# Kernel tuning notes

Measured on AMD Instinct MI355X. Metric: run time of the kernel, lower is better.

The kernel has to match this reference:

```python
import jax, jax.numpy as jnp
import numpy as np

HID = 128
H = 96
W = 96
WS = 6      # window_size
SS = 3      # shift_size
LN_EPS = 1e-5


def _layer_norm(x, g, b):
    m = x.mean(-1, keepdims=True)
    v = ((x - m) ** 2).mean(-1, keepdims=True)
    return (x - m) / jnp.sqrt(v + LN_EPS) * g + b


def _block(x, Wm, bm, g, bg):
    # Linear -> LayerNorm -> GELU (dropout is identity at inference)
    return jax.nn.gelu(_layer_norm(x @ Wm + bm, g, bg), approximate=False)


def _window_context(grid, Wt, bt, gt, bgt):
    # grid: [B, H, W, D]. Window partition + mean over the ws*ws tokens is
    # equivalent to a mean over each (ws, ws) tile; broadcasting back is a repeat.
    B, Hh, Ww, D = grid.shape
    nh, nw = Hh // WS, Ww // WS
    win_mean = grid.reshape(B, nh, WS, nw, WS, D).mean(axis=(2, 4))  # [B, nh, nw, D]
    tok = _block(win_mean, Wt, bt, gt, bgt)                          # token_proj
    return jnp.repeat(jnp.repeat(tok, WS, axis=1), WS, axis=2)       # [B, H, W, D]


def setup_inputs() -> dict:
    key = jax.random.key(0)
    ks = jax.random.split(key, 8)
    B = 32
    s = 1.0 / np.sqrt(HID)
    inp = {
        "h_pixel": jax.random.normal(ks[0], (B, H * W, HID), dtype=jnp.float32),
        "node_mask": jnp.ones((B, H * W), dtype=jnp.float32),
        # token_proj: Linear(D,D) + LayerNorm(D)
        "Wt": jax.random.normal(ks[1], (HID, HID), dtype=jnp.float32) * s,
        "bt": jnp.zeros((HID,), jnp.float32),
        "gt": jnp.ones((HID,), jnp.float32),
        "bgt": jnp.zeros((HID,), jnp.float32),
        # fuse: Linear(D,D) + LayerNorm(D)  (regular_shifted_sum -> fuse_in = D)
        "Wf": jax.random.normal(ks[2], (HID, HID), dtype=jnp.float32) * s,
        "bf": jnp.zeros((HID,), jnp.float32),
        "gf": jnp.ones((HID,), jnp.float32),
        "bgf": jnp.zeros((HID,), jnp.float32),
        # out_proj: Linear(D,D) + LayerNorm(D)
        "Wo": jax.random.normal(ks[3], (HID, HID), dtype=jnp.float32) * s,
        "bo": jnp.zeros((HID,), jnp.float32),
        "go": jnp.ones((HID,), jnp.float32),
        "bgo": jnp.zeros((HID,), jnp.float32),
    }
    return inp


def reference(h_pixel, node_mask, Wt, bt, gt, bgt, Wf, bf, gf, bgf, Wo, bo, go, bgo):
    B, N, D = h_pixel.shape
    grid = h_pixel.reshape(B, H, W, D)
    reg = _window_context(grid, Wt, bt, gt, bgt)
    shifted = jnp.roll(grid, (-SS, -SS), axis=(1, 2))
    sh = _window_context(shifted, Wt, bt, gt, bgt)
    sh = jnp.roll(sh, (SS, SS), axis=(1, 2))
    ctx = _block(reg + sh, Wf, bf, gf, bgf)     # fuse
    out = _block(ctx, Wo, bo, go, bgo)          # out_proj
    out = out.reshape(B, N, D) * node_mask[..., None]
    return out
```

## Files before the change

kernel.cpp:

```cpp
#include <hip/hip_runtime.h>
#include <hip/hip_bf16.h>


#define DEVFN static __device__ __forceinline__

typedef __attribute__((ext_vector_type(8))) short bf16x8;
typedef __attribute__((ext_vector_type(16))) float f32x16;
typedef __attribute__((ext_vector_type(2))) unsigned int uintx2;
typedef __attribute__((ext_vector_type(4))) float floatx4;

DEVFN float gelu_fast(float x) {
  const float u = 1.5957691216057308f * (x + 0.044715f * x * x * x);
  return x / (1.0f + __expf(-u));
}

DEVFN unsigned int cvt_pk_bf16(float lo, float hi) {
  unsigned int r;
  asm("v_cvt_pk_bf16_f32 %0, %1, %2" : "=v"(r) : "v"(lo), "v"(hi));
  return r;
}

DEVFN float bf2f(unsigned short u) {
  return __uint_as_float((unsigned int)u << 16);
}

DEVFN void add4(float4& a, const float4 v) {
  a.x += v.x; a.y += v.y; a.z += v.z; a.w += v.w;
}
DEVFN void fma4(float4& a, const float4 v, float m) {
  a.x = fmaf(v.x, m, a.x); a.y = fmaf(v.y, m, a.y);
  a.z = fmaf(v.z, m, a.z); a.w = fmaf(v.w, m, a.w);
}

__global__ __launch_bounds__(512) void k_tile3(const float* __restrict__ h,
                                               unsigned short* __restrict__ S3) {
  const int b  = blockIdx.x >> 5;
  const int ry = blockIdx.x & 31;
  const int w    = threadIdx.x >> 6;
  const int lane = threadIdx.x & 63;
  const int half = lane >> 5;
  const int ch4  = (lane & 31) << 2;
  const float mlo = half ? 0.f : 1.f;
  const float mhi = 1.f - mlo;

  float4 acc[4];
  #pragma unroll
  for (int t = 0; t < 4; ++t) acc[t] = make_float4(0.f, 0.f, 0.f, 0.f);

  #pragma unroll
  for (int yy = 0; yy < 3; ++yy) {
    const float* rp =
        h + ((size_t)(b * 9216 + (3 * ry + yy) * 96 + 12 * w + half) * 128 + ch4);
    #pragma unroll
    for (int j = 0; j < 6; ++j) {
      const float4 v = *reinterpret_cast<const float4*>(rp + j * 256);
      if (j == 0)      add4(acc[0], v);
      else if (j == 2) add4(acc[1], v);
      else if (j == 3) add4(acc[2], v);
      else if (j == 5) add4(acc[3], v);
      else if (j == 1) { fma4(acc[0], v, mlo); fma4(acc[1], v, mhi); }
      else             { fma4(acc[2], v, mlo); fma4(acc[3], v, mhi); }
    }
  }

  #pragma unroll
  for (int t = 0; t < 4; ++t) {
    float4 s = acc[t];
    s.x += __shfl_xor(s.x, 32, 64);
    s.y += __shfl_xor(s.y, 32, 64);
    s.z += __shfl_xor(s.z, 32, 64);
    s.w += __shfl_xor(s.w, 32, 64);
    if (half == 0) {
      uintx2 pk;
      pk.x = cvt_pk_bf16(s.x, s.y);
      pk.y = cvt_pk_bf16(s.z, s.w);
      __builtin_nontemporal_store(pk, reinterpret_cast<uintx2*>(
          &S3[((size_t)(b * 32 + ry) * 32 + 4 * w + t) * 128 + ch4]));
    }
  }
}

DEVFN void stage_w_bf(unsigned short* __restrict__ wl,
                      const float* __restrict__ W, int tid) {
  #pragma unroll
  for (int p = 0; p < 4; ++p) {
    const int i = tid + p * 512;
    const int kp = i >> 5;
    const int n4 = (i & 31) * 4;
    const float4 r0 = *reinterpret_cast<const float4*>(W + (size_t)(2 * kp) * 128 + n4);
    const float4 r1 = *reinterpret_cast<const float4*>(W + (size_t)(2 * kp + 1) * 128 + n4);
    const float a0[4] = {r0.x, r0.y, r0.z, r0.w};
    const float a1[4] = {r1.x, r1.y, r1.z, r1.w};
    #pragma unroll
    for (int j = 0; j < 4; ++j) {
      *reinterpret_cast<unsigned int*>(&wl[(n4 + j) * 136 + 2 * kp]) =
          cvt_pk_bf16(a0[j], a1[j]);
    }
  }
}

DEVFN f32x16 mfma_tile(const unsigned short* __restrict__ xrow,
                       const unsigned short* __restrict__ wrow) {
  f32x16 acc;
  #pragma unroll
  for (int r = 0; r < 16; ++r) acc[r] = 0.f;
  #pragma unroll
  for (int kk = 0; kk < 8; ++kk) {
    const bf16x8 a = *reinterpret_cast<const bf16x8*>(xrow + kk * 16);
    const bf16x8 bb = *reinterpret_cast<const bf16x8*>(wrow + kk * 16);
    acc = __builtin_amdgcn_mfma_f32_32x32x16_bf16(a, bb, acc, 0, 0, 0);
  }
  return acc;
}

DEVFN void write_raw(float* __restrict__ raw, const f32x16 acc,
                     int tg, int cg, int lane) {
  const int n  = cg * 32 + (lane & 31);
  const int mb = tg * 32 + 4 * (lane >> 5);
  #pragma unroll
  for (int r = 0; r < 16; ++r) {
    const int mm = mb + (r & 3) + 8 * (r >> 2);
    raw[mm * 132 + n] = acc[r];
  }
}

__global__ __launch_bounds__(512) void k_tok(const unsigned short* __restrict__ S3,
    const float* __restrict__ Wt, const float* __restrict__ bt,
    const float* __restrict__ gt, const float* __restrict__ bgt,
    unsigned short* __restrict__ tok) {
  __shared__ __align__(16) unsigned short xs_bf[64 * 136];
  __shared__ __align__(16) unsigned short wl[128 * 136];
  float* raw = reinterpret_cast<float*>(wl);

  const int tid = threadIdx.x;
  const int t0 = blockIdx.x * 64;
  const int s  = t0 >> 13;
  const int b  = (t0 >> 8) & 31;
  const int wyx = t0 & 255;

  const unsigned short* Sb = S3 + (size_t)b * 131072;
  #pragma unroll
  for (int p = 0; p < 2; ++p) {
    const int i = tid + p * 512;
    const int tt = i >> 4, c8 = (i & 15) * 8;
    const int idx = wyx + tt;
    const int wy = idx >> 4, wx = idx & 15;
    int ry0, ry1, c0, c1;
    if (s == 0) { ry0 = 2 * wy;     ry1 = 2 * wy + 1;        c0 = 2 * wx;     c1 = 2 * wx + 1; }
    else        { ry0 = 2 * wy + 1; ry1 = (2 * wy + 2) & 31; c0 = 2 * wx + 1; c1 = (2 * wx + 2) & 31; }
    const bf16x8 v00 = *reinterpret_cast<const bf16x8*>(Sb + ((size_t)(ry0 * 32 + c0) * 128 + c8));
    const bf16x8 v01 = *reinterpret_cast<const bf16x8*>(Sb + ((size_t)(ry0 * 32 + c1) * 128 + c8));
    const bf16x8 v10 = *reinterpret_cast<const bf16x8*>(Sb + ((size_t)(ry1 * 32 + c0) * 128 + c8));
    const bf16x8 v11 = *reinterpret_cast<const bf16x8*>(Sb + ((size_t)(ry1 * 32 + c1) * 128 + c8));
    float sv[8];
    #pragma unroll
    for (int j = 0; j < 8; ++j) {
      sv[j] = (bf2f((unsigned short)v00[j]) + bf2f((unsigned short)v01[j]) +
               bf2f((unsigned short)v10[j]) + bf2f((unsigned short)v11[j])) * (1.f / 36.f);
    }
    unsigned int* dst = reinterpret_cast<unsigned int*>(&xs_bf[tt * 136 + c8]);
    #pragma unroll
    for (int j = 0; j < 4; ++j)
      dst[j] = cvt_pk_bf16(sv[2 * j], sv[2 * j + 1]);
  }
  stage_w_bf(wl, Wt, tid);
  __syncthreads();

  const int lane = tid & 63;
  const int w = tid >> 6;
  const int tg = w >> 2, cg = w & 3;
  const unsigned short* xrow = &xs_bf[(tg * 32 + (lane & 31)) * 136 + 8 * (lane >> 5)];
  const unsigned short* wrow = &wl[(cg * 32 + (lane & 31)) * 136 + 8 * (lane >> 5)];

  const f32x16 acc = mfma_tile(xrow, wrow);
  __syncthreads();
  write_raw(raw, acc, tg, cg, lane);
  __syncthreads();

  {
    const int tt = tid >> 3, cb = tid & 7;
    float v[16];
    float s2 = 0.f, q = 0.f;
    #pragma unroll
    for (int i = 0; i < 4; ++i) {
      const int col = 4 * cb + 32 * i;
      const float4 rv = *reinterpret_cast<const float4*>(&raw[tt * 132 + col]);
      const float4 bv = *reinterpret_cast<const float4*>(bt + col);
      v[4 * i + 0] = rv.x + bv.x; v[4 * i + 1] = rv.y + bv.y;
      v[4 * i + 2] = rv.z + bv.z; v[4 * i + 3] = rv.w + bv.w;
    }
    #pragma unroll
    for (int e = 0; e < 16; ++e) { s2 += v[e]; q += v[e] * v[e]; }
    s2 += __shfl_xor(s2, 1, 8); q += __shfl_xor(q, 1, 8);
    s2 += __shfl_xor(s2, 2, 8); q += __shfl_xor(q, 2, 8);
    s2 += __shfl_xor(s2, 4, 8); q += __shfl_xor(q, 4, 8);
    const float mean = s2 * (1.f / 128.f);
    const float var  = q * (1.f / 128.f) - mean * mean;
    const float inv  = rsqrtf(var + 1e-5f);
    #pragma unroll
    for (int i = 0; i < 4; ++i) {
      const int col = 4 * cb + 32 * i;
      const float4 gv = *reinterpret_cast<const float4*>(gt + col);
      const float4 ev = *reinterpret_cast<const float4*>(bgt + col);
      const float o0 = gelu_fast((v[4 * i + 0] - mean) * inv * gv.x + ev.x);
      const float o1 = gelu_fast((v[4 * i + 1] - mean) * inv * gv.y + ev.y);
      const float o2 = gelu_fast((v[4 * i + 2] - mean) * inv * gv.z + ev.z);
      const float o3 = gelu_fast((v[4 * i + 3] - mean) * inv * gv.w + ev.w);
      uintx2 pk;
      pk.x = cvt_pk_bf16(o0, o1);
      pk.y = cvt_pk_bf16(o2, o3);
      __builtin_nontemporal_store(pk, reinterpret_cast<uintx2*>(
          tok + (size_t)(t0 + tt) * 128 + col));
    }
  }
}

__global__ __launch_bounds__(512) void k_fuse_out(const unsigned short* __restrict__ tok,
    const float* __restrict__ Wf, const float* __restrict__ bfv,
    const float* __restrict__ gf, const float* __restrict__ bgf,
    const float* __restrict__ Wo, const float* __restrict__ bo,
    const float* __restrict__ go, const float* __restrict__ bgo,
    const float* __restrict__ mask, float* __restrict__ out) {
  __shared__ __align__(16) unsigned short xs_bf[64 * 136];
  __shared__ __align__(16) unsigned short wl[128 * 136];
  float* raw = reinterpret_cast<float*>(wl);

  const int tid = threadIdx.x;
  const int b = blockIdx.x >> 4;
  const int m = blockIdx.x & 15;
  const int lane = tid & 63;
  const int w = tid >> 6;
  const int tg = w >> 2, cg = w & 3;

  const unsigned short* tokR = tok + (size_t)b * 32768 + (size_t)m * 2048;
  const unsigned short* tokS = tok + 1048576 + (size_t)b * 32768;

  #pragma unroll
  for (int p = 0; p < 2; ++p) {
    const int i = tid + p * 512;
    const int t = i >> 4, c8 = (i & 15) * 8;
    const int gx = t & 31, gy = 2 * m + (t >> 5);
    const int wx  = gx >> 1;
    const int wxs = ((gx + 31) & 31) >> 1;
    const int wys = ((gy + 31) & 31) >> 1;
    const bf16x8 pr = *reinterpret_cast<const bf16x8*>(tokR + (size_t)wx * 128 + c8);
    const bf16x8 ps = *reinterpret_cast<const bf16x8*>(tokS + (size_t)(wys * 16 + wxs) * 128 + c8);
    float sv[8];
    #pragma unroll
    for (int j = 0; j < 8; ++j)
      sv[j] = bf2f((unsigned short)pr[j]) + bf2f((unsigned short)ps[j]);
    unsigned int* dst = reinterpret_cast<unsigned int*>(&xs_bf[t * 136 + c8]);
    #pragma unroll
    for (int j = 0; j < 4; ++j)
      dst[j] = cvt_pk_bf16(sv[2 * j], sv[2 * j + 1]);
  }
  stage_w_bf(wl, Wf, tid);
  __syncthreads();

  const unsigned short* xrow = &xs_bf[(tg * 32 + (lane & 31)) * 136 + 8 * (lane >> 5)];
  const unsigned short* wrow = &wl[(cg * 32 + (lane & 31)) * 136 + 8 * (lane >> 5)];

  const f32x16 acc1 = mfma_tile(xrow, wrow);
  __syncthreads();
  write_raw(raw, acc1, tg, cg, lane);
  __syncthreads();

  {
    const int tt = tid >> 3, cb = tid & 7;
    float v[16];
    float s = 0.f, q = 0.f;
    #pragma unroll
    for (int i = 0; i < 4; ++i) {
      const int col = 4 * cb + 32 * i;
      const float4 rv = *reinterpret_cast<const float4*>(&raw[tt * 132 + col]);
      const float4 bv = *reinterpret_cast<const float4*>(bfv + col);
      v[4 * i + 0] = rv.x + bv.x; v[4 * i + 1] = rv.y + bv.y;
      v[4 * i + 2] = rv.z + bv.z; v[4 * i + 3] = rv.w + bv.w;
    }
    #pragma unroll
    for (int e = 0; e < 16; ++e) { s += v[e]; q += v[e] * v[e]; }
    s += __shfl_xor(s, 1, 8); q += __shfl_xor(q, 1, 8);
    s += __shfl_xor(s, 2, 8); q += __shfl_xor(q, 2, 8);
    s += __shfl_xor(s, 4, 8); q += __shfl_xor(q, 4, 8);
    const float mean = s * (1.f / 128.f);
    const float var  = q * (1.f / 128.f) - mean * mean;
    const float inv  = rsqrtf(var + 1e-5f);
    #pragma unroll
    for (int i = 0; i < 4; ++i) {
      const int col = 4 * cb + 32 * i;
      const float4 gv = *reinterpret_cast<const float4*>(gf + col);
      const float4 ev = *reinterpret_cast<const float4*>(bgf + col);
      const float o0 = gelu_fast((v[4 * i + 0] - mean) * inv * gv.x + ev.x);
      const float o1 = gelu_fast((v[4 * i + 1] - mean) * inv * gv.y + ev.y);
      const float o2 = gelu_fast((v[4 * i + 2] - mean) * inv * gv.z + ev.z);
      const float o3 = gelu_fast((v[4 * i + 3] - mean) * inv * gv.w + ev.w);
      uintx2 pk;
      pk.x = cvt_pk_bf16(o0, o1);
      pk.y = cvt_pk_bf16(o2, o3);
      *reinterpret_cast<uintx2*>(&xs_bf[tt * 136 + col]) = pk;
    }
  }
  __syncthreads();
  stage_w_bf(wl, Wo, tid);
  __syncthreads();

  const f32x16 acc2 = mfma_tile(xrow, wrow);
  __syncthreads();
  write_raw(raw, acc2, tg, cg, lane);
  __syncthreads();

  {
    const int tt = tid >> 3, cb = tid & 7;
    float v[16];
    float s = 0.f, q = 0.f;
    #pragma unroll
    for (int i = 0; i < 4; ++i) {
      const int col = 4 * cb + 32 * i;
      const float4 rv = *reinterpret_cast<const float4*>(&raw[tt * 132 + col]);
      const float4 bv = *reinterpret_cast<const float4*>(bo + col);
      v[4 * i + 0] = rv.x + bv.x; v[4 * i + 1] = rv.y + bv.y;
      v[4 * i + 2] = rv.z + bv.z; v[4 * i + 3] = rv.w + bv.w;
    }
    #pragma unroll
    for (int e = 0; e < 16; ++e) { s += v[e]; q += v[e] * v[e]; }
    s += __shfl_xor(s, 1, 8); q += __shfl_xor(q, 1, 8);
    s += __shfl_xor(s, 2, 8); q += __shfl_xor(q, 2, 8);
    s += __shfl_xor(s, 4, 8); q += __shfl_xor(q, 4, 8);
    const float mean = s * (1.f / 128.f);
    const float var  = q * (1.f / 128.f) - mean * mean;
    const float inv  = rsqrtf(var + 1e-5f);
    #pragma unroll
    for (int i = 0; i < 4; ++i) {
      const int col = 4 * cb + 32 * i;
      const float4 gv = *reinterpret_cast<const float4*>(go + col);
      const float4 ev = *reinterpret_cast<const float4*>(bgo + col);
      v[4 * i + 0] = gelu_fast((v[4 * i + 0] - mean) * inv * gv.x + ev.x);
      v[4 * i + 1] = gelu_fast((v[4 * i + 1] - mean) * inv * gv.y + ev.y);
      v[4 * i + 2] = gelu_fast((v[4 * i + 2] - mean) * inv * gv.z + ev.z);
      v[4 * i + 3] = gelu_fast((v[4 * i + 3] - mean) * inv * gv.w + ev.w);
    }
    const int gx = tt & 31, gy = 2 * m + (tt >> 5);
    #pragma unroll
    for (int py = 0; py < 3; ++py) {
      const int y = 3 * gy + py;
      #pragma unroll
      for (int px = 0; px < 3; ++px) {
        const int x = 3 * gx + px;
        const size_t pix = (size_t)b * 9216 + (size_t)y * 96 + x;
        const float mv = mask[pix];
        #pragma unroll
        for (int i = 0; i < 4; ++i) {
          const int col = 4 * cb + 32 * i;
          floatx4 ov;
          ov.x = v[4 * i + 0] * mv; ov.y = v[4 * i + 1] * mv;
          ov.z = v[4 * i + 2] * mv; ov.w = v[4 * i + 3] * mv;
          __builtin_nontemporal_store(ov,
              reinterpret_cast<floatx4*>(out + pix * 128 + col));
        }
      }
    }
  }
}

extern "C" void kernel_launch(void* const* d_in, const int* in_sizes, int n_in,
                              void* d_out, int out_size, void* d_ws, size_t ws_size,
                              hipStream_t stream) {
  (void)in_sizes; (void)n_in; (void)out_size; (void)ws_size;
  const float* h    = (const float*)d_in[0];
  const float* mask = (const float*)d_in[1];
  const float* Wt   = (const float*)d_in[2];
  const float* bt   = (const float*)d_in[3];
  const float* gt   = (const float*)d_in[4];
  const float* bgt  = (const float*)d_in[5];
  const float* Wf   = (const float*)d_in[6];
  const float* bfv  = (const float*)d_in[7];
  const float* gf   = (const float*)d_in[8];
  const float* bgf  = (const float*)d_in[9];
  const float* Wo   = (const float*)d_in[10];
  const float* bo   = (const float*)d_in[11];
  const float* go   = (const float*)d_in[12];
  const float* bgo  = (const float*)d_in[13];

  unsigned short* S3  = (unsigned short*)d_ws;
  unsigned short* tok = (unsigned short*)((char*)d_ws + (size_t)8 * 1024 * 1024);
  float* out = (float*)d_out;

  hipLaunchKernelGGL(k_tile3, dim3(1024), dim3(512), 0, stream, h, S3);
  hipLaunchKernelGGL(k_tok, dim3(256), dim3(512), 0, stream,
                     S3, Wt, bt, gt, bgt, tok);
  hipLaunchKernelGGL(k_fuse_out, dim3(512), dim3(512), 0, stream,
                     tok, Wf, bfv, gf, bgf, Wo, bo, go, bgo, mask, out);
}
```

Baseline: 76.35 us.

## Precompute bf16 weight images once and copy them directly into LDS

Adds three extra blocks to the first kernel that convert Wt, Wf and Wo to padded bf16 transposed images in workspace. The later kernels then copy these images straight into shared memory instead of every block reloading fp32 weights and converting them with scattered LDS writes. It also switches the large input read to nontemporal loads and replaces the GELU division with a hardware reciprocal. The cost is a small amount of extra workspace traffic and a dependency on the first kernel's extra blocks.

```diff
diff --git a/kernel.cpp b/kernel.cpp
--- a/kernel.cpp
+++ b/kernel.cpp
@@ -11,7 +11,7 @@
 
 DEVFN float gelu_fast(float x) {
   const float u = 1.5957691216057308f * (x + 0.044715f * x * x * x);
-  return x / (1.0f + __expf(-u));
+  return x * __builtin_amdgcn_rcpf(1.0f + __expf(-u));
 }
 
 DEVFN unsigned int cvt_pk_bf16(float lo, float hi) {
@@ -33,11 +33,34 @@
 }
 
 __global__ __launch_bounds__(512) void k_tile3(const float* __restrict__ h,
-                                               unsigned short* __restrict__ S3) {
+    const float* __restrict__ Wt, const float* __restrict__ Wf,
+    const float* __restrict__ Wo,
+    unsigned short* __restrict__ S3, unsigned int* __restrict__ imgs) {
+  const int tid = threadIdx.x;
+  if (blockIdx.x >= 1024) {
+    const int which = blockIdx.x - 1024;
+    const float* W = (which == 0) ? Wt : (which == 1) ? Wf : Wo;
+    unsigned int* img = imgs + (size_t)which * 8704;
+    #pragma unroll
+    for (int p = 0; p < 4; ++p) {
+      const int i = tid + p * 512;
+      const int kp = i >> 5;
+      const int n4 = (i & 31) * 4;
+      const float4 r0 = *reinterpret_cast<const float4*>(W + (size_t)(2 * kp) * 128 + n4);
+      const float4 r1 = *reinterpret_cast<const float4*>(W + (size_t)(2 * kp + 1) * 128 + n4);
+      const float a0[4] = {r0.x, r0.y, r0.z, r0.w};
+      const float a1[4] = {r1.x, r1.y, r1.z, r1.w};
+      #pragma unroll
+      for (int j = 0; j < 4; ++j)
+        img[(n4 + j) * 68 + kp] = cvt_pk_bf16(a0[j], a1[j]);
+    }
+    return;
+  }
+
   const int b  = blockIdx.x >> 5;
   const int ry = blockIdx.x & 31;
-  const int w    = threadIdx.x >> 6;
-  const int lane = threadIdx.x & 63;
+  const int w    = tid >> 6;
+  const int lane = tid & 63;
   const int half = lane >> 5;
   const int ch4  = (lane & 31) << 2;
   const float mlo = half ? 0.f : 1.f;
@@ -53,7 +76,9 @@
         h + ((size_t)(b * 9216 + (3 * ry + yy) * 96 + 12 * w + half) * 128 + ch4);
     #pragma unroll
     for (int j = 0; j < 6; ++j) {
-      const float4 v = *reinterpret_cast<const float4*>(rp + j * 256);
+      const floatx4 vv = __builtin_nontemporal_load(
+          reinterpret_cast<const floatx4*>(rp + j * 256));
+      const float4 v = make_float4(vv.x, vv.y, vv.z, vv.w);
       if (j == 0)      add4(acc[0], v);
       else if (j == 2) add4(acc[1], v);
       else if (j == 3) add4(acc[2], v);
@@ -80,23 +105,12 @@
   }
 }
 
-DEVFN void stage_w_bf(unsigned short* __restrict__ wl,
-                      const float* __restrict__ W, int tid) {
-  #pragma unroll
-  for (int p = 0; p < 4; ++p) {
-    const int i = tid + p * 512;
-    const int kp = i >> 5;
-    const int n4 = (i & 31) * 4;
-    const float4 r0 = *reinterpret_cast<const float4*>(W + (size_t)(2 * kp) * 128 + n4);
-    const float4 r1 = *reinterpret_cast<const float4*>(W + (size_t)(2 * kp + 1) * 128 + n4);
-    const float a0[4] = {r0.x, r0.y, r0.z, r0.w};
-    const float a1[4] = {r1.x, r1.y, r1.z, r1.w};
-    #pragma unroll
-    for (int j = 0; j < 4; ++j) {
-      *reinterpret_cast<unsigned int*>(&wl[(n4 + j) * 136 + 2 * kp]) =
-          cvt_pk_bf16(a0[j], a1[j]);
-    }
-  }
+DEVFN void copy_wimg(unsigned short* __restrict__ wl,
+                     const unsigned int* __restrict__ img, int tid) {
+  uint4* dst = reinterpret_cast<uint4*>(wl);
+  const uint4* src = reinterpret_cast<const uint4*>(img);
+  for (int i = tid; i < 2176; i += 512)
+    dst[i] = src[i];
 }
 
 DEVFN f32x16 mfma_tile(const unsigned short* __restrict__ xrow,
@@ -125,9 +139,9 @@
 }
 
 __global__ __launch_bounds__(512) void k_tok(const unsigned short* __restrict__ S3,
-    const float* __restrict__ Wt, const float* __restrict__ bt,
-    const float* __restrict__ gt, const float* __restrict__ bgt,
-    unsigned short* __restrict__ tok) {
+    const unsigned int* __restrict__ wimg,
+    const float* __restrict__ bt, const float* __restrict__ gt,
+    const float* __restrict__ bgt, unsigned short* __restrict__ tok) {
   __shared__ __align__(16) unsigned short xs_bf[64 * 136];
   __shared__ __align__(16) unsigned short wl[128 * 136];
   float* raw = reinterpret_cast<float*>(wl);
@@ -163,7 +177,7 @@
     for (int j = 0; j < 4; ++j)
       dst[j] = cvt_pk_bf16(sv[2 * j], sv[2 * j + 1]);
   }
-  stage_w_bf(wl, Wt, tid);
+  copy_wimg(wl, wimg, tid);
   __syncthreads();
 
   const int lane = tid & 63;
@@ -216,9 +230,9 @@
 }
 
 __global__ __launch_bounds__(512) void k_fuse_out(const unsigned short* __restrict__ tok,
-    const float* __restrict__ Wf, const float* __restrict__ bfv,
+    const unsigned int* __restrict__ wimgF, const float* __restrict__ bfv,
     const float* __restrict__ gf, const float* __restrict__ bgf,
-    const float* __restrict__ Wo, const float* __restrict__ bo,
+    const unsigned int* __restrict__ wimgO, const float* __restrict__ bo,
     const float* __restrict__ go, const float* __restrict__ bgo,
     const float* __restrict__ mask, float* __restrict__ out) {
   __shared__ __align__(16) unsigned short xs_bf[64 * 136];
@@ -254,7 +268,7 @@
     for (int j = 0; j < 4; ++j)
       dst[j] = cvt_pk_bf16(sv[2 * j], sv[2 * j + 1]);
   }
-  stage_w_bf(wl, Wf, tid);
+  copy_wimg(wl, wimgF, tid);
   __syncthreads();
 
   const unsigned short* xrow = &xs_bf[(tg * 32 + (lane & 31)) * 136 + 8 * (lane >> 5)];
@@ -301,7 +315,7 @@
     }
   }
   __syncthreads();
-  stage_w_bf(wl, Wo, tid);
+  copy_wimg(wl, wimgO, tid);
   __syncthreads();
 
   const f32x16 acc2 = mfma_tile(xrow, wrow);
@@ -383,11 +397,14 @@
 
   unsigned short* S3  = (unsigned short*)d_ws;
   unsigned short* tok = (unsigned short*)((char*)d_ws + (size_t)8 * 1024 * 1024);
+  unsigned int* imgs  = (unsigned int*)((char*)d_ws + (size_t)12 * 1024 * 1024);
   float* out = (float*)d_out;
 
-  hipLaunchKernelGGL(k_tile3, dim3(1024), dim3(512), 0, stream, h, S3);
+  hipLaunchKernelGGL(k_tile3, dim3(1027), dim3(512), 0, stream,
+                     h, Wt, Wf, Wo, S3, imgs);
   hipLaunchKernelGGL(k_tok, dim3(256), dim3(512), 0, stream,
-                     S3, Wt, bt, gt, bgt, tok);
+                     S3, imgs, bt, gt, bgt, tok);
   hipLaunchKernelGGL(k_fuse_out, dim3(512), dim3(512), 0, stream,
-                     tok, Wf, bfv, gf, bgf, Wo, bo, go, bgo, mask, out);
-}
+                     tok, imgs + 8704, bfv, gf, bgf,
+                     imgs + 17408, bo, go, bgo, mask, out);
+}
```

After: 76.31 us. No clear change (-0.1%).
